# Optimization experiments

Measured on AMD Instinct MI355X. Metric: run time of the kernel, lower is better.

The kernel has to match this reference:

```python
import jax, jax.numpy as jnp
import numpy as np

N = 100000     # nodes
E = 1600000    # edges (avg degree 16)
CI = 3         # input features (x, z, t)
W = 128        # hidden width
CO = 1         # output features
L = 4          # processor layers


def setup_inputs() -> dict:
    key = jax.random.key(0)
    ks = jax.random.split(key, 10)
    s = 0.1
    x = jax.random.normal(ks[0], (N, CI), jnp.float32)
    # compute_mask is an external geometry-dependent, no-grad mask; emulate as 0/1 node mask
    mask = (jax.random.uniform(ks[1], (N, 1)) > 0.5).astype(jnp.float32)
    edge_index = jax.random.randint(ks[2], (2, E), 0, N, dtype=jnp.int32)
    W_enc = jax.random.normal(ks[3], (CI, W), jnp.float32) * s
    b_enc = jnp.zeros((W,), jnp.float32)
    W_p = jax.random.normal(ks[4], (L, W, W), jnp.float32) * s
    b_p = jnp.zeros((L, W), jnp.float32)
    W_dec = jax.random.normal(ks[5], (W, CO), jnp.float32) * s
    b_dec = jnp.zeros((CO,), jnp.float32)
    return {"x": x, "mask": mask, "edge_index": edge_index,
            "W_enc": W_enc, "b_enc": b_enc, "W_p": W_p, "b_p": b_p,
            "W_dec": W_dec, "b_dec": b_dec}


def reference(x, mask, edge_index, W_enc, b_enc, W_p, b_p, W_dec, b_dec):
    src, dst = edge_index[0], edge_index[1]
    n = x.shape[0]
    # GCN symmetric normalization with self-loops: deg = 1 + in-degree
    deg = 1.0 + jax.ops.segment_sum(jnp.ones((src.shape[0],), x.dtype), dst, num_segments=n)
    dis = jax.lax.rsqrt(deg)                      # deg^{-1/2}, [N]
    norm = dis[src] * dis[dst]                    # [E]

    def gcn(h, Wt, b):
        h = h @ Wt                                # [N, out]
        agg = jax.ops.segment_sum(h[src] * norm[:, None], dst, num_segments=n)
        # self-loop contribution: norm_ii = dis_i^2
        return agg + h * (dis * dis)[:, None] + b

    h = jax.nn.relu(gcn(x, W_enc, b_enc))
    for l in range(L):
        h = jax.nn.relu(gcn(h, W_p[l], b_p[l]))
    out = gcn(h, W_dec, b_dec)
    return out * mask
```

## Files before the change

### kernel.cpp

```cpp
#include <hip/hip_runtime.h>
#include <hip/hip_fp16.h>


#define HW 128
#define NBMAX 1024
#define CAP 4096

typedef _Float16 f16x8 __attribute__((ext_vector_type(8)));
typedef float f32x4 __attribute__((ext_vector_type(4)));

__global__ void k_zero_i32(int* __restrict__ a, int n) {
    int i = blockIdx.x * 256 + threadIdx.x;
    if (i < n) a[i] = 0;
}

__global__ __launch_bounds__(256) void k_histb(const int* __restrict__ dstA,
                                               int* __restrict__ bcnt,
                                               int nb, int e, int nblk) {
    __shared__ int lh[NBMAX];
    for (int b = threadIdx.x; b < nb; b += 256) lh[b] = 0;
    __syncthreads();
    int blk = blockIdx.x;
    int c0 = (int)(((long long)e * blk) / nblk);
    int c1 = (int)(((long long)e * (blk + 1)) / nblk);
    for (int i = c0 + threadIdx.x; i < c1; i += 256) atomicAdd(&lh[dstA[i] >> 7], 1);
    __syncthreads();
    for (int b = threadIdx.x; b < nb; b += 256) {
        int v = lh[b];
        if (v) atomicAdd(&bcnt[b], v);
    }
}

__global__ void k_bscan(const int* __restrict__ bcnt, int* __restrict__ bstart,
                        int* __restrict__ bcur, int nb, int etot) {
    __shared__ int s[1024];
    int t = threadIdx.x;
    int d0 = (t < nb) ? bcnt[t] : 0;
    s[t] = d0;
    __syncthreads();
    for (int off = 1; off < 1024; off <<= 1) {
        int v = (t >= off) ? s[t - off] : 0;
        __syncthreads();
        s[t] += v;
        __syncthreads();
    }
    if (t < nb) {
        int ex = s[t] - d0;
        bstart[t] = ex;
        bcur[t] = ex;
    }
    if (t == 0) bstart[nb] = etot;
}

__global__ __launch_bounds__(256) void k_part(const int* __restrict__ srcA,
                                              const int* __restrict__ dstA,
                                              int* __restrict__ bcur,
                                              unsigned* __restrict__ stage,
                                              int nb, int e, int nblk) {
    __shared__ int lh[NBMAX];
    __shared__ int loff[NBMAX];
    for (int b = threadIdx.x; b < nb; b += 256) lh[b] = 0;
    __syncthreads();
    int blk = blockIdx.x;
    int c0 = (int)(((long long)e * blk) / nblk);
    int c1 = (int)(((long long)e * (blk + 1)) / nblk);
    for (int i = c0 + threadIdx.x; i < c1; i += 256) atomicAdd(&lh[dstA[i] >> 7], 1);
    __syncthreads();
    for (int b = threadIdx.x; b < nb; b += 256) {
        int v = lh[b];
        loff[b] = v ? atomicAdd(&bcur[b], v) : 0;
    }
    __syncthreads();
    for (int b = threadIdx.x; b < nb; b += 256) lh[b] = 0;
    __syncthreads();
    for (int i = c0 + threadIdx.x; i < c1; i += 256) {
        int d = dstA[i];
        int bk = d >> 7;
        int p = loff[bk] + atomicAdd(&lh[bk], 1);
        stage[p] = ((unsigned)srcA[i] << 7) | (unsigned)(d & 127);
    }
}

__global__ __launch_bounds__(256) void k_build(const unsigned* __restrict__ stage,
                                               const int* __restrict__ bstart,
                                               const float* __restrict__ x,
                                               int* __restrict__ row_start,
                                               float* __restrict__ dis,
                                               float4* __restrict__ x4,
                                               int* __restrict__ csr, int n, int nb) {
    __shared__ int lcnt[128];
    __shared__ int sc[128];
    __shared__ int lcsr[CAP];
    int b = blockIdx.x, tid = threadIdx.x;
    int base = bstart[b], end = bstart[b + 1], cnt = end - base;
    int node0 = b << 7;

    if (tid < 128) lcnt[tid] = 0;
    __syncthreads();
    for (int j = tid; j < cnt; j += 256) atomicAdd(&lcnt[stage[base + j] & 127], 1);
    __syncthreads();
    if (tid < 128) sc[tid] = lcnt[tid];
    __syncthreads();
    for (int off = 1; off < 128; off <<= 1) {
        int v = (tid < 128 && tid >= off) ? sc[tid - off] : 0;
        __syncthreads();
        if (tid < 128) sc[tid] += v;
        __syncthreads();
    }
    int node = node0 + tid;
    if (tid < 128 && node < n) {
        int excl = sc[tid] - lcnt[tid];
        row_start[node] = base + excl;
        float dv = rsqrtf(1.f + (float)lcnt[tid]);
        dis[node] = dv;
        x4[node] = make_float4(x[node * 3] * dv, x[node * 3 + 1] * dv,
                               x[node * 3 + 2] * dv, 0.f);
    }
    if (tid == 0 && b == nb - 1) row_start[n] = end;
    __syncthreads();
    if (tid < 128) sc[tid] = sc[tid] - lcnt[tid];
    __syncthreads();
    if (tid < 128) lcnt[tid] = 0;
    __syncthreads();
    if (cnt <= CAP) {
        for (int j = tid; j < cnt; j += 256) {
            unsigned v = stage[base + j];
            int dl = v & 127;
            int p = atomicAdd(&lcnt[dl], 1);
            lcsr[sc[dl] + p] = (int)(v >> 7);
        }
        __syncthreads();
        for (int j = tid; j < cnt; j += 256) csr[base + j] = lcsr[j];
    } else {
        for (int j = tid; j < cnt; j += 256) {
            unsigned v = stage[base + j];
            int dl = v & 127;
            int p = atomicAdd(&lcnt[dl], 1);
            csr[base + sc[dl] + p] = (int)(v >> 7);
        }
    }
}

__global__ void k_prep_wt(const float* __restrict__ Wp, __half* __restrict__ WTh,
                          __half* __restrict__ WTl, int total) {
    int t = blockIdx.x * 256 + threadIdx.x;
    if (t >= total) return;
    int l = t >> 14;
    int kc = t & 16383;
    int k = kc >> 7, c = kc & 127;
    float w = Wp[t];
    __half hi = __float2half_rn(w);
    __half lo = __float2half_rn(w - __half2float(hi));
    size_t o = ((size_t)l << 14) + (size_t)c * HW + k;
    WTh[o] = hi;
    WTl[o] = lo;
}

__global__ void k_enc_agg(const float4* __restrict__ x4, const int* __restrict__ rs,
                          const int* __restrict__ csr, const float* __restrict__ dis,
                          float4* __restrict__ zx, int n) {
    int i = blockIdx.x * 256 + threadIdx.x;
    if (i >= n) return;
    float4 a = x4[i];
    int e1 = rs[i + 1];
    for (int j = rs[i]; j < e1; ++j) {
        float4 v = x4[csr[j]];
        a.x += v.x; a.y += v.y; a.z += v.z;
    }
    float d = dis[i];
    zx[i] = make_float4(a.x * d, a.y * d, a.z * d, 0.f);
}

__global__ void k_enc_gemm(const float4* __restrict__ zx, const float* __restrict__ We,
                           const float* __restrict__ be, const float* __restrict__ dis,
                           __half* __restrict__ H, int n) {
    int t = blockIdx.x * 256 + threadIdx.x;
    int i = t >> 7;
    int c = t & 127;
    if (i >= n) return;
    float4 z = zx[i];
    float v = z.x * We[c] + z.y * We[HW + c] + z.z * We[2 * HW + c] + be[c];
    H[(size_t)i * HW + c] = __float2half_rn(fmaxf(v, 0.f) * dis[i]);
}

__global__ __launch_bounds__(256) void k_agg128(const __half* __restrict__ Hin,
                                                const int* __restrict__ rs,
                                                const int* __restrict__ csr,
                                                const float* __restrict__ dis,
                                                __half* __restrict__ Z, int n) {
    int wave = threadIdx.x >> 6, lane = threadIdx.x & 63;
    int lg = lane & 15;
    int node = (blockIdx.x * 4 + wave) * 4 + (lane >> 4);
    bool active = node < n;

    float a0[8], a1[8], a2[8], a3[8];
#pragma unroll
    for (int j = 0; j < 8; ++j) { a0[j] = 0.f; a1[j] = 0.f; a2[j] = 0.f; a3[j] = 0.f; }

    int e0 = 0, e1 = 0;
    if (active) {
        e0 = rs[node];
        e1 = rs[node + 1];
        f16x8 hv = *(const f16x8*)(Hin + (size_t)node * HW + lg * 8);
#pragma unroll
        for (int j = 0; j < 8; ++j) a0[j] = (float)hv[j];
    }

    for (int base = e0; base < e1; base += 16) {
        int cnt = e1 - base;
        if (cnt > 16) cnt = 16;
        int sl = (base + lg < e1) ? csr[base + lg] : 0;
        int k = 0;
        for (; k + 4 <= cnt; k += 4) {
            int s0 = __shfl(sl, k + 0, 16);
            int s1 = __shfl(sl, k + 1, 16);
            int s2 = __shfl(sl, k + 2, 16);
            int s3 = __shfl(sl, k + 3, 16);
            f16x8 v0 = *(const f16x8*)(Hin + (size_t)s0 * HW + lg * 8);
            f16x8 v1 = *(const f16x8*)(Hin + (size_t)s1 * HW + lg * 8);
            f16x8 v2 = *(const f16x8*)(Hin + (size_t)s2 * HW + lg * 8);
            f16x8 v3 = *(const f16x8*)(Hin + (size_t)s3 * HW + lg * 8);
#pragma unroll
            for (int j = 0; j < 8; ++j) {
                a0[j] += (float)v0[j];
                a1[j] += (float)v1[j];
                a2[j] += (float)v2[j];
                a3[j] += (float)v3[j];
            }
        }
        for (; k < cnt; ++k) {
            int s = __shfl(sl, k, 16);
            f16x8 v = *(const f16x8*)(Hin + (size_t)s * HW + lg * 8);
#pragma unroll
            for (int j = 0; j < 8; ++j) a0[j] += (float)v[j];
        }
    }

    if (active) {
        float d = dis[node];
        union { uint4 u; __half2 h[4]; } pk;
#pragma unroll
        for (int j = 0; j < 4; ++j) {
            float lo = d * ((a0[2 * j] + a1[2 * j]) + (a2[2 * j] + a3[2 * j]));
            float hi = d * ((a0[2 * j + 1] + a1[2 * j + 1]) + (a2[2 * j + 1] + a3[2 * j + 1]));
            pk.h[j] = __floats2half2_rn(lo, hi);
        }
        *(uint4*)(Z + (size_t)node * HW + lg * 8) = pk.u;
    }
}

#define GBM 256
__global__ __launch_bounds__(256) void k_gemm_mfma(const __half* __restrict__ Z,
                                                   const __half* __restrict__ WTh,
                                                   const __half* __restrict__ WTl,
                                                   const float* __restrict__ b,
                                                   const float* __restrict__ dis,
                                                   __half* __restrict__ Hout,
                                                   const float* __restrict__ Wd,
                                                   float* __restrict__ tout,
                                                   int mode, int n) {
    int wave = threadIdx.x >> 6, lane = threadIdx.x & 63;
    int q = lane >> 4, r16 = lane & 15;
    int row0 = blockIdx.x * GBM + wave * 64;

    f32x4 acc[4][8];
#pragma unroll
    for (int mt = 0; mt < 4; ++mt)
#pragma unroll
        for (int nt = 0; nt < 8; ++nt) acc[mt][nt] = (f32x4)0.f;

#pragma unroll
    for (int ks = 0; ks < 4; ++ks) {
        f16x8 afr[4];
#pragma unroll
        for (int mt = 0; mt < 4; ++mt) {
            int row = row0 + mt * 16 + r16;
            row = row < n ? row : (n - 1);
            afr[mt] = *(const f16x8*)(Z + (size_t)row * HW + ks * 32 + q * 8);
        }
#pragma unroll
        for (int nt = 0; nt < 8; ++nt) {
            f16x8 bh = *(const f16x8*)(WTh + (size_t)(nt * 16 + r16) * HW + ks * 32 + q * 8);
            f16x8 bl = *(const f16x8*)(WTl + (size_t)(nt * 16 + r16) * HW + ks * 32 + q * 8);
#pragma unroll
            for (int mt = 0; mt < 4; ++mt) {
                acc[mt][nt] = __builtin_amdgcn_mfma_f32_16x16x32_f16(afr[mt], bh, acc[mt][nt], 0, 0, 0);
                acc[mt][nt] = __builtin_amdgcn_mfma_f32_16x16x32_f16(afr[mt], bl, acc[mt][nt], 0, 0, 0);
            }
        }
    }

    float dr[4][4];
#pragma unroll
    for (int mt = 0; mt < 4; ++mt)
#pragma unroll
        for (int r = 0; r < 4; ++r) {
            int row = row0 + mt * 16 + q * 4 + r;
            dr[mt][r] = (row < n) ? dis[row] : 0.f;
        }
    float bias[8];
#pragma unroll
    for (int nt = 0; nt < 8; ++nt) bias[nt] = b[nt * 16 + r16];

    if (mode == 0) {
#pragma unroll
        for (int nt = 0; nt < 8; ++nt) {
#pragma unroll
            for (int mt = 0; mt < 4; ++mt) {
#pragma unroll
                for (int r = 0; r < 4; ++r) {
                    int row = row0 + mt * 16 + q * 4 + r;
                    if (row < n) {
                        float v = fmaxf(acc[mt][nt][r] + bias[nt], 0.f) * dr[mt][r];
                        Hout[(size_t)row * HW + nt * 16 + r16] = __float2half_rn(v);
                    }
                }
            }
        }
    } else {
        float wd[8];
#pragma unroll
        for (int nt = 0; nt < 8; ++nt) wd[nt] = Wd[nt * 16 + r16];
#pragma unroll
        for (int mt = 0; mt < 4; ++mt) {
#pragma unroll
            for (int r = 0; r < 4; ++r) {
                float pr = 0.f;
#pragma unroll
                for (int nt = 0; nt < 8; ++nt)
                    pr += fmaxf(acc[mt][nt][r] + bias[nt], 0.f) * wd[nt];
                pr *= dr[mt][r];
#pragma unroll
                for (int off = 1; off < 16; off <<= 1) pr += __shfl_xor(pr, off, 16);
                if (r16 == 0) {
                    int row = row0 + mt * 16 + q * 4 + r;
                    if (row < n) tout[row] = pr;
                }
            }
        }
    }
}

__global__ void k_dec_out(const float* __restrict__ t, const int* __restrict__ rs,
                          const int* __restrict__ csr, const float* __restrict__ dis,
                          const float* __restrict__ bdec, const float* __restrict__ mask,
                          float* __restrict__ out, int n) {
    int i = blockIdx.x * 256 + threadIdx.x;
    if (i >= n) return;
    float acc = t[i];
    int e1 = rs[i + 1];
    for (int j = rs[i]; j < e1; ++j) acc += t[csr[j]];
    out[i] = (dis[i] * acc + bdec[0]) * mask[i];
}

static inline size_t align256(size_t x) { return (x + 255) & ~(size_t)255; }

extern "C" void kernel_launch(void* const* d_in, const int* in_sizes, int n_in,
                              void* d_out, int out_size, void* d_ws, size_t ws_size,
                              hipStream_t stream) {
    const float* x     = (const float*)d_in[0];
    const float* mask  = (const float*)d_in[1];
    const int*   ei    = (const int*)d_in[2];
    const float* W_enc = (const float*)d_in[3];
    const float* b_enc = (const float*)d_in[4];
    const float* W_p   = (const float*)d_in[5];
    const float* b_p   = (const float*)d_in[6];
    const float* W_dec = (const float*)d_in[7];
    const float* b_dec = (const float*)d_in[8];

    const int N = in_sizes[1];
    const int E = in_sizes[2] / 2;
    const int* srcA = ei;
    const int* dstA = ei + E;
    const int NB = (N + 127) >> 7;

    char* p = (char*)d_ws;
    size_t off = 0;
    auto carve = [&](size_t bytes) {
        void* r = p + off;
        off += align256(bytes);
        return r;
    };
    int*      bcnt      = (int*)carve((size_t)NB * 4);
    int*      bstart    = (int*)carve((size_t)(NB + 1) * 4);
    int*      bcur      = (int*)carve((size_t)NB * 4);
    int*      row_start = (int*)carve((size_t)(N + 1) * 4);
    unsigned* stage     = (unsigned*)carve((size_t)E * 4);
    int*      csr       = (int*)carve((size_t)E * 4);
    float*    dis       = (float*)carve((size_t)N * 4);
    float4*   x4        = (float4*)carve((size_t)N * 16);
    float4*   zx        = (float4*)carve((size_t)N * 16);
    float*    tdec      = (float*)carve((size_t)N * 4);
    __half*   WTh       = (__half*)carve((size_t)4 * HW * HW * 2);
    __half*   WTl       = (__half*)carve((size_t)4 * HW * HW * 2);
    __half*   HA        = (__half*)carve((size_t)N * HW * 2);
    __half*   HB        = (__half*)carve((size_t)N * HW * 2);

    const int gN    = (N + 255) / 256;
    const int gAgg  = (N + 15) / 16;
    const int gG    = (N + GBM - 1) / GBM;
    const int WPT   = 4 * HW * HW;
    const int PBLK  = 256;

    k_zero_i32<<<(NB + 255) / 256, 256, 0, stream>>>(bcnt, NB);
    k_histb<<<PBLK, 256, 0, stream>>>(dstA, bcnt, NB, E, PBLK);
    k_bscan<<<1, 1024, 0, stream>>>(bcnt, bstart, bcur, NB, E);
    k_part<<<PBLK, 256, 0, stream>>>(srcA, dstA, bcur, stage, NB, E, PBLK);
    k_build<<<NB, 256, 0, stream>>>(stage, bstart, x, row_start, dis, x4, csr, N, NB);
    k_prep_wt<<<(WPT + 255) / 256, 256, 0, stream>>>(W_p, WTh, WTl, WPT);

    k_enc_agg<<<gN, 256, 0, stream>>>(x4, row_start, csr, dis, zx, N);
    k_enc_gemm<<<(N * HW + 255) / 256, 256, 0, stream>>>(zx, W_enc, b_enc, dis, HA, N);

    __half* Hin = HA;
    __half* Hoth = HB;
    for (int l = 0; l < 4; ++l) {
        k_agg128<<<gAgg, 256, 0, stream>>>(Hin, row_start, csr, dis, Hoth, N);
        int mode = (l == 3) ? 1 : 0;
        k_gemm_mfma<<<gG, 256, 0, stream>>>(Hoth, WTh + (size_t)l * HW * HW,
                                            WTl + (size_t)l * HW * HW,
                                            b_p + (size_t)l * HW, dis, Hoth,
                                            W_dec, tdec, mode, N);
        __half* t = Hin; Hin = Hoth; Hoth = t;
    }

    k_dec_out<<<gN, 256, 0, stream>>>(tdec, row_start, csr, dis, b_dec, mask,
                                      (float*)d_out, N);
}
```

Before: 514.0 us.

## Store hidden features in column-sliced layout and degree-sort nodes for aggregation

Hidden activations move from row-major [N,128] to eight 16-column slices [8][N][16]. Aggregation runs one block per (128-node chunk, slice), so each slice's gather working set (about 3.2MB) is more likely to stay in cache. k_build also writes a per-chunk permutation that orders nodes by in-degree, which keeps lanes in a wave on similar edge counts and reduces divergence. In exchange, each edge's CSR index is read once per slice, eight times in total, and the GEMM A-loads and outputs must use the strided sliced addressing.

```diff
diff --git a/kernel.cpp b/kernel.cpp
--- a/kernel.cpp
+++ b/kernel.cpp
@@ -87,19 +87,25 @@
                                                int* __restrict__ row_start,
                                                float* __restrict__ dis,
                                                float4* __restrict__ x4,
-                                               int* __restrict__ csr, int n, int nb) {
+                                               int* __restrict__ csr,
+                                               int* __restrict__ perm,
+                                               int n, int nb) {
     __shared__ int lcnt[128];
     __shared__ int sc[128];
+    __shared__ int dbin[64];
     __shared__ int lcsr[CAP];
     int b = blockIdx.x, tid = threadIdx.x;
     int base = bstart[b], end = bstart[b + 1], cnt = end - base;
     int node0 = b << 7;
 
     if (tid < 128) lcnt[tid] = 0;
+    if (tid < 64) dbin[tid] = 0;
+    if (tid < 128) perm[(b << 7) + tid] = -1;
     __syncthreads();
     for (int j = tid; j < cnt; j += 256) atomicAdd(&lcnt[stage[base + j] & 127], 1);
     __syncthreads();
-    if (tid < 128) sc[tid] = lcnt[tid];
+    int mydeg = (tid < 128) ? lcnt[tid] : 0;
+    if (tid < 128) sc[tid] = mydeg;
     __syncthreads();
     for (int off = 1; off < 128; off <<= 1) {
         int v = (tid < 128 && tid >= off) ? sc[tid - off] : 0;
@@ -108,18 +114,30 @@
         __syncthreads();
     }
     int node = node0 + tid;
-    if (tid < 128 && node < n) {
-        int excl = sc[tid] - lcnt[tid];
+    bool valid = (tid < 128 && node < n);
+    if (valid) {
+        int excl = sc[tid] - mydeg;
         row_start[node] = base + excl;
-        float dv = rsqrtf(1.f + (float)lcnt[tid]);
+        float dv = rsqrtf(1.f + (float)mydeg);
         dis[node] = dv;
         x4[node] = make_float4(x[node * 3] * dv, x[node * 3 + 1] * dv,
                                x[node * 3 + 2] * dv, 0.f);
+        atomicAdd(&dbin[mydeg < 63 ? mydeg : 63], 1);
     }
     if (tid == 0 && b == nb - 1) row_start[n] = end;
     __syncthreads();
-    if (tid < 128) sc[tid] = sc[tid] - lcnt[tid];
-    __syncthreads();
+    if (tid == 0) {
+        int s = 0;
+#pragma unroll
+        for (int i = 0; i < 64; ++i) { int c = dbin[i]; dbin[i] = s; s += c; }
+    }
+    __syncthreads();
+    if (valid) {
+        int r = atomicAdd(&dbin[mydeg < 63 ? mydeg : 63], 1);
+        perm[(b << 7) + r] = node;
+    }
+    __syncthreads();
+    if (tid < 128) sc[tid] = sc[tid] - mydeg;
     if (tid < 128) lcnt[tid] = 0;
     __syncthreads();
     if (cnt <= CAP) {
@@ -180,63 +198,65 @@
     if (i >= n) return;
     float4 z = zx[i];
     float v = z.x * We[c] + z.y * We[HW + c] + z.z * We[2 * HW + c] + be[c];
-    H[(size_t)i * HW + c] = __float2half_rn(fmaxf(v, 0.f) * dis[i]);
-}
-
-__global__ __launch_bounds__(256) void k_agg128(const __half* __restrict__ Hin,
+    H[((size_t)(c >> 4) * n + i) * 16 + (c & 15)] = __float2half_rn(fmaxf(v, 0.f) * dis[i]);
+}
+
+__global__ __launch_bounds__(256) void k_agg_sl(const __half* __restrict__ Hin,
                                                 const int* __restrict__ rs,
                                                 const int* __restrict__ csr,
+                                                const int* __restrict__ perm,
                                                 const float* __restrict__ dis,
                                                 __half* __restrict__ Z, int n) {
-    int wave = threadIdx.x >> 6, lane = threadIdx.x & 63;
-    int lg = lane & 15;
-    int node = (blockIdx.x * 4 + wave) * 4 + (lane >> 4);
-    bool active = node < n;
+    int s = blockIdx.x & 7;
+    int chunk = blockIdx.x >> 3;
+    int lane = threadIdx.x & 63, wave = threadIdx.x >> 6;
+    int lg = lane & 1;
+    int node = perm[(chunk << 7) + (wave << 5) + (lane >> 1)];
+    const __half* Hs = Hin + (size_t)s * n * 16;
 
     float a0[8], a1[8], a2[8], a3[8];
 #pragma unroll
     for (int j = 0; j < 8; ++j) { a0[j] = 0.f; a1[j] = 0.f; a2[j] = 0.f; a3[j] = 0.f; }
 
     int e0 = 0, e1 = 0;
-    if (active) {
+    if (node >= 0) {
         e0 = rs[node];
         e1 = rs[node + 1];
-        f16x8 hv = *(const f16x8*)(Hin + (size_t)node * HW + lg * 8);
+        f16x8 hv = *(const f16x8*)(Hs + (size_t)node * 16 + lg * 8);
 #pragma unroll
         for (int j = 0; j < 8; ++j) a0[j] = (float)hv[j];
     }
 
-    for (int base = e0; base < e1; base += 16) {
+    for (int base = e0; base < e1; base += 8) {
         int cnt = e1 - base;
-        if (cnt > 16) cnt = 16;
-        int sl = (base + lg < e1) ? csr[base + lg] : 0;
-        int k = 0;
-        for (; k + 4 <= cnt; k += 4) {
-            int s0 = __shfl(sl, k + 0, 16);
-            int s1 = __shfl(sl, k + 1, 16);
-            int s2 = __shfl(sl, k + 2, 16);
-            int s3 = __shfl(sl, k + 3, 16);
-            f16x8 v0 = *(const f16x8*)(Hin + (size_t)s0 * HW + lg * 8);
-            f16x8 v1 = *(const f16x8*)(Hin + (size_t)s1 * HW + lg * 8);
-            f16x8 v2 = *(const f16x8*)(Hin + (size_t)s2 * HW + lg * 8);
-            f16x8 v3 = *(const f16x8*)(Hin + (size_t)s3 * HW + lg * 8);
-#pragma unroll
-            for (int j = 0; j < 8; ++j) {
-                a0[j] += (float)v0[j];
-                a1[j] += (float)v1[j];
-                a2[j] += (float)v2[j];
-                a3[j] += (float)v3[j];
-            }
-        }
-        for (; k < cnt; ++k) {
-            int s = __shfl(sl, k, 16);
-            f16x8 v = *(const f16x8*)(Hin + (size_t)s * HW + lg * 8);
-#pragma unroll
-            for (int j = 0; j < 8; ++j) a0[j] += (float)v[j];
-        }
-    }
-
-    if (active) {
+        if (cnt > 8) cnt = 8;
+        int sA0 = (base + 0 + lg < e1) ? csr[base + 0 + lg] : 0;
+        int sA1 = (base + 2 + lg < e1) ? csr[base + 2 + lg] : 0;
+        int sA2 = (base + 4 + lg < e1) ? csr[base + 4 + lg] : 0;
+        int sA3 = (base + 6 + lg < e1) ? csr[base + 6 + lg] : 0;
+        int m0 = __shfl(sA0, 0, 2), m1 = __shfl(sA0, 1, 2);
+        int m2 = __shfl(sA1, 0, 2), m3 = __shfl(sA1, 1, 2);
+        int m4 = __shfl(sA2, 0, 2), m5 = __shfl(sA2, 1, 2);
+        int m6 = __shfl(sA3, 0, 2), m7 = __shfl(sA3, 1, 2);
+        f16x8 z8 = (f16x8)(_Float16)0.f;
+        f16x8 v0 = (0 < cnt) ? *(const f16x8*)(Hs + (size_t)m0 * 16 + lg * 8) : z8;
+        f16x8 v1 = (1 < cnt) ? *(const f16x8*)(Hs + (size_t)m1 * 16 + lg * 8) : z8;
+        f16x8 v2 = (2 < cnt) ? *(const f16x8*)(Hs + (size_t)m2 * 16 + lg * 8) : z8;
+        f16x8 v3 = (3 < cnt) ? *(const f16x8*)(Hs + (size_t)m3 * 16 + lg * 8) : z8;
+        f16x8 v4 = (4 < cnt) ? *(const f16x8*)(Hs + (size_t)m4 * 16 + lg * 8) : z8;
+        f16x8 v5 = (5 < cnt) ? *(const f16x8*)(Hs + (size_t)m5 * 16 + lg * 8) : z8;
+        f16x8 v6 = (6 < cnt) ? *(const f16x8*)(Hs + (size_t)m6 * 16 + lg * 8) : z8;
+        f16x8 v7 = (7 < cnt) ? *(const f16x8*)(Hs + (size_t)m7 * 16 + lg * 8) : z8;
+#pragma unroll
+        for (int j = 0; j < 8; ++j) {
+            a0[j] += (float)v0[j]; a1[j] += (float)v1[j];
+            a2[j] += (float)v2[j]; a3[j] += (float)v3[j];
+            a0[j] += (float)v4[j]; a1[j] += (float)v5[j];
+            a2[j] += (float)v6[j]; a3[j] += (float)v7[j];
+        }
+    }
+
+    if (node >= 0) {
         float d = dis[node];
         union { uint4 u; __half2 h[4]; } pk;
 #pragma unroll
@@ -245,7 +265,7 @@
             float hi = d * ((a0[2 * j + 1] + a1[2 * j + 1]) + (a2[2 * j + 1] + a3[2 * j + 1]));
             pk.h[j] = __floats2half2_rn(lo, hi);
         }
-        *(uint4*)(Z + (size_t)node * HW + lg * 8) = pk.u;
+        *(uint4*)(Z + ((size_t)s * n + node) * 16 + lg * 8) = pk.u;
     }
 }
 
@@ -271,12 +291,14 @@
 
 #pragma unroll
     for (int ks = 0; ks < 4; ++ks) {
+        int asl = 2 * ks + (q >> 1);
+        int aoff = (q & 1) * 8;
         f16x8 afr[4];
 #pragma unroll
         for (int mt = 0; mt < 4; ++mt) {
             int row = row0 + mt * 16 + r16;
             row = row < n ? row : (n - 1);
-            afr[mt] = *(const f16x8*)(Z + (size_t)row * HW + ks * 32 + q * 8);
+            afr[mt] = *(const f16x8*)(Z + ((size_t)asl * n + row) * 16 + aoff);
         }
 #pragma unroll
         for (int nt = 0; nt < 8; ++nt) {
@@ -312,7 +334,7 @@
                     int row = row0 + mt * 16 + q * 4 + r;
                     if (row < n) {
                         float v = fmaxf(acc[mt][nt][r] + bias[nt], 0.f) * dr[mt][r];
-                        Hout[(size_t)row * HW + nt * 16 + r16] = __float2half_rn(v);
+                        Hout[((size_t)nt * n + row) * 16 + r16] = __float2half_rn(v);
                     }
                 }
             }
@@ -385,6 +407,7 @@
     int*      bstart    = (int*)carve((size_t)(NB + 1) * 4);
     int*      bcur      = (int*)carve((size_t)NB * 4);
     int*      row_start = (int*)carve((size_t)(N + 1) * 4);
+    int*      perm      = (int*)carve((size_t)NB * 128 * 4);
     unsigned* stage     = (unsigned*)carve((size_t)E * 4);
     int*      csr       = (int*)carve((size_t)E * 4);
     float*    dis       = (float*)carve((size_t)N * 4);
@@ -396,17 +419,16 @@
     __half*   HA        = (__half*)carve((size_t)N * HW * 2);
     __half*   HB        = (__half*)carve((size_t)N * HW * 2);
 
-    const int gN    = (N + 255) / 256;
-    const int gAgg  = (N + 15) / 16;
-    const int gG    = (N + GBM - 1) / GBM;
-    const int WPT   = 4 * HW * HW;
-    const int PBLK  = 256;
+    const int gN   = (N + 255) / 256;
+    const int gG   = (N + GBM - 1) / GBM;
+    const int WPT  = 4 * HW * HW;
+    const int PBLK = 256;
 
     k_zero_i32<<<(NB + 255) / 256, 256, 0, stream>>>(bcnt, NB);
     k_histb<<<PBLK, 256, 0, stream>>>(dstA, bcnt, NB, E, PBLK);
     k_bscan<<<1, 1024, 0, stream>>>(bcnt, bstart, bcur, NB, E);
     k_part<<<PBLK, 256, 0, stream>>>(srcA, dstA, bcur, stage, NB, E, PBLK);
-    k_build<<<NB, 256, 0, stream>>>(stage, bstart, x, row_start, dis, x4, csr, N, NB);
+    k_build<<<NB, 256, 0, stream>>>(stage, bstart, x, row_start, dis, x4, csr, perm, N, NB);
     k_prep_wt<<<(WPT + 255) / 256, 256, 0, stream>>>(W_p, WTh, WTl, WPT);
 
     k_enc_agg<<<gN, 256, 0, stream>>>(x4, row_start, csr, dis, zx, N);
@@ -415,7 +437,7 @@
     __half* Hin = HA;
     __half* Hoth = HB;
     for (int l = 0; l < 4; ++l) {
-        k_agg128<<<gAgg, 256, 0, stream>>>(Hin, row_start, csr, dis, Hoth, N);
+        k_agg_sl<<<8 * NB, 256, 0, stream>>>(Hin, row_start, csr, perm, dis, Hoth, N);
         int mode = (l == 3) ? 1 : 0;
         k_gemm_mfma<<<gG, 256, 0, stream>>>(Hoth, WTh + (size_t)l * HW * HW,
                                             WTl + (size_t)l * HW * HW,
```

After: 610.9 us. +18.8%, slower.

## Sort nodes by degree within each 128-node bucket for aggregation balance

Applied to the files above, without the earlier changes.

The CSR build kernel now counting-sorts the nodes of each 128-node bucket by in-degree and writes a permutation array. The aggregation kernel reads its node from this permutation, so the four nodes handled by each wave have similar degrees and fewer lanes sit idle waiting on the longest neighbour list. The cost is an extra permutation load per group, less contiguous row access across groups, and more shared-memory atomics and a serial scan in the build kernel.

```diff
diff --git a/kernel.cpp b/kernel.cpp
--- a/kernel.cpp
+++ b/kernel.cpp
@@ -87,19 +87,25 @@
                                                int* __restrict__ row_start,
                                                float* __restrict__ dis,
                                                float4* __restrict__ x4,
-                                               int* __restrict__ csr, int n, int nb) {
+                                               int* __restrict__ csr,
+                                               int* __restrict__ perm,
+                                               int n, int nb) {
     __shared__ int lcnt[128];
     __shared__ int sc[128];
+    __shared__ int dbin[64];
     __shared__ int lcsr[CAP];
     int b = blockIdx.x, tid = threadIdx.x;
     int base = bstart[b], end = bstart[b + 1], cnt = end - base;
     int node0 = b << 7;
 
     if (tid < 128) lcnt[tid] = 0;
+    if (tid < 64) dbin[tid] = 0;
+    if (tid < 128) perm[(b << 7) + tid] = -1;
     __syncthreads();
     for (int j = tid; j < cnt; j += 256) atomicAdd(&lcnt[stage[base + j] & 127], 1);
     __syncthreads();
-    if (tid < 128) sc[tid] = lcnt[tid];
+    int mydeg = (tid < 128) ? lcnt[tid] : 0;
+    if (tid < 128) sc[tid] = mydeg;
     __syncthreads();
     for (int off = 1; off < 128; off <<= 1) {
         int v = (tid < 128 && tid >= off) ? sc[tid - off] : 0;
@@ -108,18 +114,30 @@
         __syncthreads();
     }
     int node = node0 + tid;
-    if (tid < 128 && node < n) {
-        int excl = sc[tid] - lcnt[tid];
+    bool valid = (tid < 128 && node < n);
+    if (valid) {
+        int excl = sc[tid] - mydeg;
         row_start[node] = base + excl;
-        float dv = rsqrtf(1.f + (float)lcnt[tid]);
+        float dv = rsqrtf(1.f + (float)mydeg);
         dis[node] = dv;
         x4[node] = make_float4(x[node * 3] * dv, x[node * 3 + 1] * dv,
                                x[node * 3 + 2] * dv, 0.f);
+        atomicAdd(&dbin[mydeg < 63 ? mydeg : 63], 1);
     }
     if (tid == 0 && b == nb - 1) row_start[n] = end;
     __syncthreads();
-    if (tid < 128) sc[tid] = sc[tid] - lcnt[tid];
-    __syncthreads();
+    if (tid == 0) {
+        int s = 0;
+#pragma unroll
+        for (int i = 0; i < 64; ++i) { int c = dbin[i]; dbin[i] = s; s += c; }
+    }
+    __syncthreads();
+    if (valid) {
+        int r = atomicAdd(&dbin[mydeg < 63 ? mydeg : 63], 1);
+        perm[(b << 7) + r] = node;
+    }
+    __syncthreads();
+    if (tid < 128) sc[tid] = sc[tid] - mydeg;
     if (tid < 128) lcnt[tid] = 0;
     __syncthreads();
     if (cnt <= CAP) {
@@ -186,12 +204,14 @@
 __global__ __launch_bounds__(256) void k_agg128(const __half* __restrict__ Hin,
                                                 const int* __restrict__ rs,
                                                 const int* __restrict__ csr,
+                                                const int* __restrict__ perm,
                                                 const float* __restrict__ dis,
                                                 __half* __restrict__ Z, int n) {
     int wave = threadIdx.x >> 6, lane = threadIdx.x & 63;
     int lg = lane & 15;
-    int node = (blockIdx.x * 4 + wave) * 4 + (lane >> 4);
-    bool active = node < n;
+    int idx = (blockIdx.x * 4 + wave) * 4 + (lane >> 4);
+    int node = perm[idx];
+    bool active = node >= 0;
 
     float a0[8], a1[8], a2[8], a3[8];
 #pragma unroll
@@ -385,6 +405,7 @@
     int*      bstart    = (int*)carve((size_t)(NB + 1) * 4);
     int*      bcur      = (int*)carve((size_t)NB * 4);
     int*      row_start = (int*)carve((size_t)(N + 1) * 4);
+    int*      perm      = (int*)carve((size_t)NB * 128 * 4);
     unsigned* stage     = (unsigned*)carve((size_t)E * 4);
     int*      csr       = (int*)carve((size_t)E * 4);
     float*    dis       = (float*)carve((size_t)N * 4);
@@ -396,17 +417,17 @@
     __half*   HA        = (__half*)carve((size_t)N * HW * 2);
     __half*   HB        = (__half*)carve((size_t)N * HW * 2);
 
-    const int gN    = (N + 255) / 256;
-    const int gAgg  = (N + 15) / 16;
-    const int gG    = (N + GBM - 1) / GBM;
-    const int WPT   = 4 * HW * HW;
-    const int PBLK  = 256;
+    const int gN   = (N + 255) / 256;
+    const int gAgg = (NB * 128) / 16;
+    const int gG   = (N + GBM - 1) / GBM;
+    const int WPT  = 4 * HW * HW;
+    const int PBLK = 256;
 
     k_zero_i32<<<(NB + 255) / 256, 256, 0, stream>>>(bcnt, NB);
     k_histb<<<PBLK, 256, 0, stream>>>(dstA, bcnt, NB, E, PBLK);
     k_bscan<<<1, 1024, 0, stream>>>(bcnt, bstart, bcur, NB, E);
     k_part<<<PBLK, 256, 0, stream>>>(srcA, dstA, bcur, stage, NB, E, PBLK);
-    k_build<<<NB, 256, 0, stream>>>(stage, bstart, x, row_start, dis, x4, csr, N, NB);
+    k_build<<<NB, 256, 0, stream>>>(stage, bstart, x, row_start, dis, x4, csr, perm, N, NB);
     k_prep_wt<<<(WPT + 255) / 256, 256, 0, stream>>>(W_p, WTh, WTl, WPT);
 
     k_enc_agg<<<gN, 256, 0, stream>>>(x4, row_start, csr, dis, zx, N);
@@ -415,7 +436,7 @@
     __half* Hin = HA;
     __half* Hoth = HB;
     for (int l = 0; l < 4; ++l) {
-        k_agg128<<<gAgg, 256, 0, stream>>>(Hin, row_start, csr, dis, Hoth, N);
+        k_agg128<<<gAgg, 256, 0, stream>>>(Hin, row_start, csr, perm, dis, Hoth, N);
         int mode = (l == 3) ? 1 : 0;
         k_gemm_mfma<<<gG, 256, 0, stream>>>(Hoth, WTh + (size_t)l * HW * HW,
                                             WTl + (size_t)l * HW * HW,
```

Result: slower. 574.8 us (+11.8%).

## Precompute per-block partition offsets and unroll aggregation gather by eight

Applied to the files above, without the earlier changes.

The histogram kernel now stores per-block bucket counts, and a new column-scan kernel turns them into deterministic per-block write offsets. This lets the partition kernel skip its second histogram pass and its global atomics on bucket cursors. The aggregation loop also gains an 8-wide unrolled gather so more neighbor loads are in flight per iteration, and one redundant barrier is removed in the build kernel. The cost is an extra kernel launch, two PBLK×NB scratch arrays, and higher register pressure in the aggregation kernel.

```diff
diff --git a/kernel.cpp b/kernel.cpp
--- a/kernel.cpp
+++ b/kernel.cpp
@@ -5,6 +5,7 @@
 #define HW 128
 #define NBMAX 1024
 #define CAP 4096
+#define PBLK 256
 
 typedef _Float16 f16x8 __attribute__((ext_vector_type(8)));
 typedef float f32x4 __attribute__((ext_vector_type(4)));
@@ -16,6 +17,7 @@
 
 __global__ __launch_bounds__(256) void k_histb(const int* __restrict__ dstA,
                                                int* __restrict__ bcnt,
+                                               int* __restrict__ pcnt,
                                                int nb, int e, int nblk) {
     __shared__ int lh[NBMAX];
     for (int b = threadIdx.x; b < nb; b += 256) lh[b] = 0;
@@ -27,12 +29,13 @@
     __syncthreads();
     for (int b = threadIdx.x; b < nb; b += 256) {
         int v = lh[b];
+        pcnt[(size_t)blk * nb + b] = v;
         if (v) atomicAdd(&bcnt[b], v);
     }
 }
 
 __global__ void k_bscan(const int* __restrict__ bcnt, int* __restrict__ bstart,
-                        int* __restrict__ bcur, int nb, int etot) {
+                        int nb, int etot) {
     __shared__ int s[1024];
     int t = threadIdx.x;
     int d0 = (t < nb) ? bcnt[t] : 0;
@@ -44,35 +47,42 @@
         s[t] += v;
         __syncthreads();
     }
-    if (t < nb) {
-        int ex = s[t] - d0;
-        bstart[t] = ex;
-        bcur[t] = ex;
-    }
+    if (t < nb) bstart[t] = s[t] - d0;
     if (t == 0) bstart[nb] = etot;
+}
+
+__global__ __launch_bounds__(PBLK) void k_soff2(const int* __restrict__ pcnt,
+                                                const int* __restrict__ bstart,
+                                                int* __restrict__ soff, int nb) {
+    __shared__ int s[PBLK];
+    int b = blockIdx.x, t = threadIdx.x;
+    int v = pcnt[(size_t)t * nb + b];
+    s[t] = v;
+    __syncthreads();
+    for (int off = 1; off < PBLK; off <<= 1) {
+        int u = (t >= off) ? s[t - off] : 0;
+        __syncthreads();
+        s[t] += u;
+        __syncthreads();
+    }
+    soff[(size_t)t * nb + b] = bstart[b] + s[t] - v;
 }
 
 __global__ __launch_bounds__(256) void k_part(const int* __restrict__ srcA,
                                               const int* __restrict__ dstA,
-                                              int* __restrict__ bcur,
+                                              const int* __restrict__ soff,
                                               unsigned* __restrict__ stage,
                                               int nb, int e, int nblk) {
+    __shared__ int loff[NBMAX];
     __shared__ int lh[NBMAX];
-    __shared__ int loff[NBMAX];
-    for (int b = threadIdx.x; b < nb; b += 256) lh[b] = 0;
-    __syncthreads();
     int blk = blockIdx.x;
+    for (int b = threadIdx.x; b < nb; b += 256) {
+        loff[b] = soff[(size_t)blk * nb + b];
+        lh[b] = 0;
+    }
+    __syncthreads();
     int c0 = (int)(((long long)e * blk) / nblk);
     int c1 = (int)(((long long)e * (blk + 1)) / nblk);
-    for (int i = c0 + threadIdx.x; i < c1; i += 256) atomicAdd(&lh[dstA[i] >> 7], 1);
-    __syncthreads();
-    for (int b = threadIdx.x; b < nb; b += 256) {
-        int v = lh[b];
-        loff[b] = v ? atomicAdd(&bcur[b], v) : 0;
-    }
-    __syncthreads();
-    for (int b = threadIdx.x; b < nb; b += 256) lh[b] = 0;
-    __syncthreads();
     for (int i = c0 + threadIdx.x; i < c1; i += 256) {
         int d = dstA[i];
         int bk = d >> 7;
@@ -119,7 +129,6 @@
     if (tid == 0 && b == nb - 1) row_start[n] = end;
     __syncthreads();
     if (tid < 128) sc[tid] = sc[tid] - lcnt[tid];
-    __syncthreads();
     if (tid < 128) lcnt[tid] = 0;
     __syncthreads();
     if (cnt <= CAP) {
@@ -211,6 +220,35 @@
         if (cnt > 16) cnt = 16;
         int sl = (base + lg < e1) ? csr[base + lg] : 0;
         int k = 0;
+        for (; k + 8 <= cnt; k += 8) {
+            int s0 = __shfl(sl, k + 0, 16);
+            int s1 = __shfl(sl, k + 1, 16);
+            int s2 = __shfl(sl, k + 2, 16);
+            int s3 = __shfl(sl, k + 3, 16);
+            int s4 = __shfl(sl, k + 4, 16);
+            int s5 = __shfl(sl, k + 5, 16);
+            int s6 = __shfl(sl, k + 6, 16);
+            int s7 = __shfl(sl, k + 7, 16);
+            f16x8 v0 = *(const f16x8*)(Hin + (size_t)s0 * HW + lg * 8);
+            f16x8 v1 = *(const f16x8*)(Hin + (size_t)s1 * HW + lg * 8);
+            f16x8 v2 = *(const f16x8*)(Hin + (size_t)s2 * HW + lg * 8);
+            f16x8 v3 = *(const f16x8*)(Hin + (size_t)s3 * HW + lg * 8);
+            f16x8 v4 = *(const f16x8*)(Hin + (size_t)s4 * HW + lg * 8);
+            f16x8 v5 = *(const f16x8*)(Hin + (size_t)s5 * HW + lg * 8);
+            f16x8 v6 = *(const f16x8*)(Hin + (size_t)s6 * HW + lg * 8);
+            f16x8 v7 = *(const f16x8*)(Hin + (size_t)s7 * HW + lg * 8);
+#pragma unroll
+            for (int j = 0; j < 8; ++j) {
+                a0[j] += (float)v0[j];
+                a1[j] += (float)v1[j];
+                a2[j] += (float)v2[j];
+                a3[j] += (float)v3[j];
+                a0[j] += (float)v4[j];
+                a1[j] += (float)v5[j];
+                a2[j] += (float)v6[j];
+                a3[j] += (float)v7[j];
+            }
+        }
         for (; k + 4 <= cnt; k += 4) {
             int s0 = __shfl(sl, k + 0, 16);
             int s1 = __shfl(sl, k + 1, 16);
@@ -383,7 +421,8 @@
     };
     int*      bcnt      = (int*)carve((size_t)NB * 4);
     int*      bstart    = (int*)carve((size_t)(NB + 1) * 4);
-    int*      bcur      = (int*)carve((size_t)NB * 4);
+    int*      pcnt      = (int*)carve((size_t)PBLK * NB * 4);
+    int*      soff      = (int*)carve((size_t)PBLK * NB * 4);
     int*      row_start = (int*)carve((size_t)(N + 1) * 4);
     unsigned* stage     = (unsigned*)carve((size_t)E * 4);
     int*      csr       = (int*)carve((size_t)E * 4);
@@ -396,16 +435,16 @@
     __half*   HA        = (__half*)carve((size_t)N * HW * 2);
     __half*   HB        = (__half*)carve((size_t)N * HW * 2);
 
-    const int gN    = (N + 255) / 256;
-    const int gAgg  = (N + 15) / 16;
-    const int gG    = (N + GBM - 1) / GBM;
-    const int WPT   = 4 * HW * HW;
-    const int PBLK  = 256;
+    const int gN   = (N + 255) / 256;
+    const int gAgg = (N + 15) / 16;
+    const int gG   = (N + GBM - 1) / GBM;
+    const int WPT  = 4 * HW * HW;
 
     k_zero_i32<<<(NB + 255) / 256, 256, 0, stream>>>(bcnt, NB);
-    k_histb<<<PBLK, 256, 0, stream>>>(dstA, bcnt, NB, E, PBLK);
-    k_bscan<<<1, 1024, 0, stream>>>(bcnt, bstart, bcur, NB, E);
-    k_part<<<PBLK, 256, 0, stream>>>(srcA, dstA, bcur, stage, NB, E, PBLK);
+    k_histb<<<PBLK, 256, 0, stream>>>(dstA, bcnt, pcnt, NB, E, PBLK);
+    k_bscan<<<1, 1024, 0, stream>>>(bcnt, bstart, NB, E);
+    k_soff2<<<NB, PBLK, 0, stream>>>(pcnt, bstart, soff, NB);
+    k_part<<<PBLK, 256, 0, stream>>>(srcA, dstA, soff, stage, NB, E, PBLK);
     k_build<<<NB, 256, 0, stream>>>(stage, bstart, x, row_start, dis, x4, csr, N, NB);
     k_prep_wt<<<(WPT + 255) / 256, 256, 0, stream>>>(W_p, WTh, WTl, WPT);
 
```

Result: slower. 531.7 us (+3.4%).
